# Optimization experiments

Hardware: AMD Instinct MI355X
Metric: run time of the kernel (lower is better)

The kernel has to match this reference:

```python
import jax, jax.numpy as jnp
import numpy as np
import math

DIM = 1024
HEADS = 16
HEAD_DIM = DIM // HEADS
FFN = 4096
B, S = 2, 2048
EPS = 1e-12


def layernorm(x, w, b):
    u = jnp.mean(x, axis=-1, keepdims=True)
    s = jnp.mean((x - u) ** 2, axis=-1, keepdims=True)
    return w * ((x - u) / jnp.sqrt(s + EPS)) + b


def setup_inputs() -> dict:
    key = jax.random.key(0)
    ks = jax.random.split(key, 8)
    scale = 0.02
    return {
        "x": jax.random.normal(ks[0], (B, S, DIM), dtype=jnp.float32),
        "mask": jnp.zeros((1, 1, S, S), dtype=jnp.float32),
        "wq": jax.random.normal(ks[1], (DIM, DIM), dtype=jnp.float32) * scale,
        "wk": jax.random.normal(ks[2], (DIM, DIM), dtype=jnp.float32) * scale,
        "wv": jax.random.normal(ks[3], (DIM, DIM), dtype=jnp.float32) * scale,
        "wo": jax.random.normal(ks[4], (DIM, DIM), dtype=jnp.float32) * scale,
        "w1": jax.random.normal(ks[5], (DIM, FFN), dtype=jnp.float32) * scale,
        "w2": jax.random.normal(ks[6], (FFN, DIM), dtype=jnp.float32) * scale,
        "ln1_w": jnp.ones((DIM,), dtype=jnp.float32),
        "ln1_b": jnp.zeros((DIM,), dtype=jnp.float32),
        "ln2_w": jnp.ones((DIM,), dtype=jnp.float32),
        "ln2_b": jnp.zeros((DIM,), dtype=jnp.float32),
    }


def reference(x, mask, wq, wk, wv, wo, w1, w2, ln1_w, ln1_b, ln2_w, ln2_b):
    # --- attention sub-block (pre-LN) ---
    h = layernorm(x, ln1_w, ln1_b)
    q = (h @ wq).reshape(B, S, HEADS, HEAD_DIM).transpose(0, 2, 1, 3)  # [B,H,S,D]
    k = (h @ wk).reshape(B, S, HEADS, HEAD_DIM).transpose(0, 2, 1, 3)
    v = (h @ wv).reshape(B, S, HEADS, HEAD_DIM).transpose(0, 2, 1, 3)
    scores = jnp.einsum("bhsd,bhtd->bhst", q, k) / math.sqrt(HEAD_DIM)
    scores = scores + mask
    probs = jax.nn.softmax(scores.astype(jnp.float32), axis=-1).astype(q.dtype)
    attn = jnp.einsum("bhst,bhtd->bhsd", probs, v)  # [B,H,S,D]
    attn = attn.transpose(0, 2, 1, 3).reshape(B, S, DIM)
    x = x + attn @ wo
    # --- FFN sub-block (pre-LN) ---
    h = layernorm(x, ln2_w, ln2_b)
    m = jax.nn.gelu(h @ w1, approximate=False) @ w2
    return x + m
```

## Files before the change

kernel.cpp:

```cpp
#include <hip/hip_runtime.h>
#include <math.h>


#define DIMSZ 1024
#define SEQ   2048
#define BATCH 2
#define NHEAD 16
#define HD    64
#define FFNSZ 4096
#define ROWS  (BATCH*SEQ)

typedef __attribute__((ext_vector_type(8))) short bf8_t;
typedef __attribute__((ext_vector_type(4))) float f4_t;

__device__ __forceinline__ unsigned short f2bf(float f) {
  union { float f; unsigned u; } c; c.f = f;
  unsigned u = c.u;
  return (unsigned short)((u + 0x7fffu + ((u >> 16) & 1u)) >> 16);
}

__device__ __forceinline__ float fast_exp2(float x) {
#if __has_builtin(__builtin_amdgcn_exp2f)
  return __builtin_amdgcn_exp2f(x);
#else
  return exp2f(x);
#endif
}

__device__ __forceinline__ unsigned int pk_trunc_bf16(float a, float b) {
#if __has_builtin(__builtin_amdgcn_perm)
  return __builtin_amdgcn_perm(__float_as_uint(b), __float_as_uint(a), 0x07060302u);
#else
  return (__float_as_uint(b) & 0xffff0000u) | (__float_as_uint(a) >> 16);
#endif
}

__device__ __forceinline__ void async16(const void* g, void* l) {
  __builtin_amdgcn_global_load_lds((const __attribute__((address_space(1))) void*)g,
                                   (__attribute__((address_space(3))) void*)l,
                                   16, 0, 0);
}

__device__ __forceinline__ f4_t mfma_bf16(bf8_t a, bf8_t b, f4_t c) {
  return __builtin_amdgcn_mfma_f32_16x16x32_bf16(a, b, c, 0, 0, 0);
}

__global__ __launch_bounds__(256) void ln_kernel(const float* __restrict__ x,
                                                 const float* __restrict__ w,
                                                 const float* __restrict__ b,
                                                 unsigned short* __restrict__ out) {
  int row  = blockIdx.x * 4 + (threadIdx.x >> 6);
  int lane = threadIdx.x & 63;
  const float4* xr = (const float4*)(x + (size_t)row * DIMSZ);
  float4 v[4];
  float s = 0.f, s2 = 0.f;
#pragma unroll
  for (int i = 0; i < 4; ++i) {
    v[i] = xr[lane + 64*i];
    s  += (v[i].x + v[i].y) + (v[i].z + v[i].w);
    s2 += (v[i].x*v[i].x + v[i].y*v[i].y) + (v[i].z*v[i].z + v[i].w*v[i].w);
  }
#pragma unroll
  for (int off = 32; off; off >>= 1) {
    s  += __shfl_xor(s,  off);
    s2 += __shfl_xor(s2, off);
  }
  float mean = s * (1.f/DIMSZ);
  float var  = s2 * (1.f/DIMSZ) - mean*mean;
  float rstd = rsqrtf(var + 1e-12f);
  const float4* wr = (const float4*)w;
  const float4* br = (const float4*)b;
#pragma unroll
  for (int i = 0; i < 4; ++i) {
    float4 wv = wr[lane + 64*i];
    float4 bv = br[lane + 64*i];
    ushort4 o;
    o.x = f2bf((v[i].x - mean) * rstd * wv.x + bv.x);
    o.y = f2bf((v[i].y - mean) * rstd * wv.y + bv.y);
    o.z = f2bf((v[i].z - mean) * rstd * wv.z + bv.z);
    o.w = f2bf((v[i].w - mean) * rstd * wv.w + bv.w);
    *(ushort4*)(out + (size_t)row * DIMSZ + (size_t)(lane + 64*i) * 4) = o;
  }
}

__global__ __launch_bounds__(256) void wtrans4_kernel(const float* __restrict__ w0,
                                                      const float* __restrict__ w1,
                                                      const float* __restrict__ w2,
                                                      const float* __restrict__ w3,
                                                      unsigned short* __restrict__ o0,
                                                      unsigned short* __restrict__ o1,
                                                      unsigned short* __restrict__ o2,
                                                      unsigned short* __restrict__ o3) {
  const int K = 1024, N = 1024;
  const float* w = (blockIdx.z == 0) ? w0 : (blockIdx.z == 1) ? w1 : (blockIdx.z == 2) ? w2 : w3;
  unsigned short* wT = (blockIdx.z == 0) ? o0 : (blockIdx.z == 1) ? o1 : (blockIdx.z == 2) ? o2 : o3;
  __shared__ float t[32][33];
  int tx = threadIdx.x & 31, ty = threadIdx.x >> 5;
  int n0 = blockIdx.x * 32, k0 = blockIdx.y * 32;
#pragma unroll
  for (int i = 0; i < 4; ++i)
    t[ty + 8*i][tx] = w[(size_t)(k0 + ty + 8*i) * N + n0 + tx];
  __syncthreads();
#pragma unroll
  for (int i = 0; i < 4; ++i)
    wT[(size_t)(n0 + ty + 8*i) * K + k0 + tx] = f2bf(t[tx][ty + 8*i]);
}

__global__ __launch_bounds__(256) void wtrans_kernel(const float* __restrict__ w,
                                                     unsigned short* __restrict__ wT,
                                                     int K, int N) {
  __shared__ float t[32][33];
  int tx = threadIdx.x & 31, ty = threadIdx.x >> 5;
  int n0 = blockIdx.x * 32, k0 = blockIdx.y * 32;
#pragma unroll
  for (int i = 0; i < 4; ++i)
    t[ty + 8*i][tx] = w[(size_t)(k0 + ty + 8*i) * N + n0 + tx];
  __syncthreads();
#pragma unroll
  for (int i = 0; i < 4; ++i)
    wT[(size_t)(n0 + ty + 8*i) * K + k0 + tx] = f2bf(t[tx][ty + 8*i]);
}

__global__ __launch_bounds__(256) void vt_kernel(const unsigned short* __restrict__ qkv,
                                                 unsigned short* __restrict__ vt) {
  __shared__ unsigned short tile[64][65];
  int bh = blockIdx.y, b = bh >> 4, h = bh & 15;
  int s0 = blockIdx.x * 64;
  int tx = threadIdx.x & 63, ty = threadIdx.x >> 6;
#pragma unroll
  for (int i = 0; i < 16; ++i) {
    int s = ty + i*4;
    tile[s][tx] = qkv[((size_t)(b*SEQ) + s0 + s) * 3072 + 2048 + h*HD + tx];
  }
  __syncthreads();
#pragma unroll
  for (int i = 0; i < 16; ++i) {
    int d = ty + i*4;
    vt[((size_t)bh * HD + d) * SEQ + s0 + tx] = tile[tx][d];
  }
}

template<int EPI>
__global__ __launch_bounds__(256) void gemm_bt(const unsigned short* __restrict__ A,
                                               const unsigned short* __restrict__ Bt,
                                               void* __restrict__ Cv,
                                               const float* __restrict__ res,
                                               int M, int N, int K) {
  __shared__ unsigned short As[128*32];
  __shared__ unsigned short Bs[128*32];
  int tid  = threadIdx.x;
  int wv   = tid >> 6, lane = tid & 63, quad = lane >> 4, ml = lane & 15;
  int wrow = (wv >> 1) * 64, wcol = (wv & 1) * 64;
  const unsigned short* Ab = A  + (size_t)blockIdx.y * 128 * K;
  const unsigned short* Bb = Bt + (size_t)blockIdx.x * 128 * K;

  f4_t acc[4][4];
#pragma unroll
  for (int i = 0; i < 4; ++i)
#pragma unroll
    for (int j = 0; j < 4; ++j) acc[i][j] = (f4_t){0.f, 0.f, 0.f, 0.f};

  int r0 = tid >> 2, c0 = (tid & 3) * 8;

  for (int k0 = 0; k0 < K; k0 += 32) {
    async16(Ab + (size_t)r0 * K + k0 + c0,        &As[(size_t)tid * 8]);
    async16(Ab + (size_t)(r0+64) * K + k0 + c0,   &As[((size_t)tid + 256) * 8]);
    async16(Bb + (size_t)r0 * K + k0 + c0,        &Bs[(size_t)tid * 8]);
    async16(Bb + (size_t)(r0+64) * K + k0 + c0,   &Bs[((size_t)tid + 256) * 8]);
    __syncthreads();

    bf8_t af[4], bfr[4];
#pragma unroll
    for (int i = 0; i < 4; ++i)
      af[i] = *(const bf8_t*)(&As[(wrow + i*16 + ml) * 32 + quad * 8]);
#pragma unroll
    for (int j = 0; j < 4; ++j)
      bfr[j] = *(const bf8_t*)(&Bs[(wcol + j*16 + ml) * 32 + quad * 8]);
#pragma unroll
    for (int i = 0; i < 4; ++i)
#pragma unroll
      for (int j = 0; j < 4; ++j)
        acc[i][j] = mfma_bf16(af[i], bfr[j], acc[i][j]);
    __syncthreads();
  }

#pragma unroll
  for (int i = 0; i < 4; ++i) {
    int grow = blockIdx.y * 128 + wrow + i*16 + quad*4;
#pragma unroll
    for (int j = 0; j < 4; ++j) {
      int gcol = blockIdx.x * 128 + wcol + j*16 + ml;
#pragma unroll
      for (int r = 0; r < 4; ++r) {
        size_t off = (size_t)(grow + r) * N + gcol;
        float v = acc[i][j][r];
        if constexpr (EPI == 2) {
          ((float*)Cv)[off] = res[off] + v;
        } else {
          if constexpr (EPI == 1)
            v = 0.5f * v * (1.f + erff(v * 0.70710678118654752f));
          ((unsigned short*)Cv)[off] = f2bf(v);
        }
      }
    }
  }
}

__global__ __launch_bounds__(256) void attn_kernel(const unsigned short* __restrict__ qkv,
                                                   const unsigned short* __restrict__ vt,
                                                   const float* __restrict__ mask,
                                                   unsigned short* __restrict__ attnout) {
  __shared__ unsigned short Ks[2][2][64][32];
  __shared__ unsigned short Vs[2][2][64][32];
  __shared__ unsigned short Ps[4][16][72];

  int bh = blockIdx.y, b = bh >> 4, h = bh & 15;
  int tid = threadIdx.x;
  int wv = tid >> 6, lane = tid & 63;
  int quad = lane >> 4, ml = lane & 15;
  int q0 = blockIdx.x * 64;
  int q  = q0 + wv * 16 + ml;

  const unsigned short* qrow = qkv + ((size_t)(b*SEQ) + q) * 3072 + h*HD;
  bf8_t qf0 = *(const bf8_t*)(qrow + quad*8);
  bf8_t qf1 = *(const bf8_t*)(qrow + 32 + quad*8);

  const unsigned short* kbase = qkv + (size_t)(b*SEQ) * 3072 + DIMSZ + h*HD;
  const unsigned short* vbase = vt + (size_t)bh * HD * SEQ;
  const float* mrow = mask + (size_t)q * SEQ;

  int srow = tid >> 2;
  int scol = (tid & 3) * 8;

  f4_t O[4];
#pragma unroll
  for (int dt = 0; dt < 4; ++dt) O[dt] = (f4_t){0.f, 0.f, 0.f, 0.f};
  float lR = 0.f;

  const float C1 = 0.18033688011112042f;
  const float C2 = 1.4426950408889634f;

  auto stage = [&](int t0, int buf) {
#pragma unroll
    for (int dh = 0; dh < 2; ++dh)
      async16(kbase + (size_t)(t0 + srow) * 3072 + dh*32 + scol,
              &Ks[buf][dh][0][0] + (size_t)tid * 8);
#pragma unroll
    for (int kc = 0; kc < 2; ++kc)
      async16(vbase + (size_t)srow * SEQ + t0 + kc*32 + scol,
              &Vs[buf][kc][0][0] + (size_t)tid * 8);
  };
  auto loadmask = [&](int t0, float4* mv) {
#pragma unroll
    for (int mt = 0; mt < 4; ++mt)
      mv[mt] = *(const float4*)(mrow + t0 + mt*16 + quad*4);
  };
  auto compute = [&](int buf, const float4* mv) {
#pragma unroll
    for (int mt = 0; mt < 4; ++mt) {
      bf8_t kf0 = *(const bf8_t*)(&Ks[buf][0][mt*16 + ml][quad*8]);
      bf8_t kf1 = *(const bf8_t*)(&Ks[buf][1][mt*16 + ml][quad*8]);
      f4_t s = (f4_t){0.f, 0.f, 0.f, 0.f};
      s = mfma_bf16(kf0, qf0, s);
      s = mfma_bf16(kf1, qf1, s);
      float p0 = fast_exp2(fmaf(s[0], C1, mv[mt].x * C2));
      float p1 = fast_exp2(fmaf(s[1], C1, mv[mt].y * C2));
      float p2 = fast_exp2(fmaf(s[2], C1, mv[mt].z * C2));
      float p3 = fast_exp2(fmaf(s[3], C1, mv[mt].w * C2));
      lR += (p0 + p1) + (p2 + p3);
      uint2 pk;
      pk.x = pk_trunc_bf16(p0, p1);
      pk.y = pk_trunc_bf16(p2, p3);
      *(uint2*)(&Ps[wv][ml][mt*16 + quad*4]) = pk;
    }
#pragma unroll
    for (int kc = 0; kc < 2; ++kc) {
      bf8_t pf = *(const bf8_t*)(&Ps[wv][ml][kc*32 + quad*8]);
#pragma unroll
      for (int dt = 0; dt < 4; ++dt) {
        bf8_t vf = *(const bf8_t*)(&Vs[buf][kc][dt*16 + ml][quad*8]);
        O[dt] = mfma_bf16(vf, pf, O[dt]);
      }
    }
  };

  float4 mcur[4], mnxt[4];
  stage(0, 0);
  loadmask(0, mcur);

#pragma unroll 1
  for (int c = 0; c < SEQ/64; c += 2) {
    __syncthreads();
    loadmask((c+1)*64, mnxt);
    stage((c+1)*64, 1);
    compute(0, mcur);
    __syncthreads();
    if (c + 2 < SEQ/64) {
      loadmask((c+2)*64, mcur);
      stage((c+2)*64, 0);
    }
    compute(1, mnxt);
  }

  lR += __shfl_xor(lR, 16);
  lR += __shfl_xor(lR, 32);
  float linv = 1.f / lR;
#pragma unroll
  for (int dt = 0; dt < 4; ++dt) {
    ushort4 o;
    o.x = f2bf(O[dt][0] * linv);
    o.y = f2bf(O[dt][1] * linv);
    o.z = f2bf(O[dt][2] * linv);
    o.w = f2bf(O[dt][3] * linv);
    *(ushort4*)(attnout + ((size_t)(b*SEQ) + q) * DIMSZ + h*HD + dt*16 + quad*4) = o;
  }
}

extern "C" void kernel_launch(void* const* d_in, const int* in_sizes, int n_in,
                              void* d_out, int out_size, void* d_ws, size_t ws_size,
                              hipStream_t stream) {
  const float* x    = (const float*)d_in[0];
  const float* mask = (const float*)d_in[1];
  const float* wq   = (const float*)d_in[2];
  const float* wk   = (const float*)d_in[3];
  const float* wvp  = (const float*)d_in[4];
  const float* wo   = (const float*)d_in[5];
  const float* w1   = (const float*)d_in[6];
  const float* w2   = (const float*)d_in[7];
  const float* ln1w = (const float*)d_in[8];
  const float* ln1b = (const float*)d_in[9];
  const float* ln2w = (const float*)d_in[10];
  const float* ln2b = (const float*)d_in[11];
  float* out = (float*)d_out;

  char* ws = (char*)d_ws;
  unsigned short* wqkvT  = (unsigned short*)(ws + 0);
  unsigned short* woT    = (unsigned short*)(ws + 6291456);
  unsigned short* w1T    = (unsigned short*)(ws + 8388608);
  unsigned short* w2T    = (unsigned short*)(ws + 16777216);
  unsigned short* attno  = (unsigned short*)(ws + 25165824);
  float*          x2     = (float*)         (ws + 33554432);
  unsigned short* hbuf   = (unsigned short*)(ws + 50331648);
  unsigned short* qkvb   = (unsigned short*)(ws + 58720256);
  unsigned short* vtb    = (unsigned short*)(ws + 83886080);
  unsigned short* gbuf   = (unsigned short*)(ws + 58720256);

  ln_kernel<<<ROWS/4, 256, 0, stream>>>(x, ln1w, ln1b, hbuf);
  wtrans4_kernel<<<dim3(32, 32, 4), 256, 0, stream>>>(wq, wk, wvp, wo,
      wqkvT, wqkvT + 1024*1024, wqkvT + 2*1024*1024, woT);
  wtrans_kernel<<<dim3(128, 32), 256, 0, stream>>>(w1, w1T, 1024, 4096);
  wtrans_kernel<<<dim3(32, 128), 256, 0, stream>>>(w2, w2T, 4096, 1024);
  gemm_bt<0><<<dim3(3072/128, 4096/128), 256, 0, stream>>>(hbuf, wqkvT, qkvb, nullptr, ROWS, 3072, 1024);
  vt_kernel<<<dim3(SEQ/64, BATCH*NHEAD), 256, 0, stream>>>(qkvb, vtb);
  attn_kernel<<<dim3(SEQ/64, BATCH*NHEAD), 256, 0, stream>>>(qkvb, vtb, mask, attno);
  gemm_bt<2><<<dim3(1024/128, 4096/128), 256, 0, stream>>>(attno, woT, x2, x, ROWS, 1024, 1024);
  ln_kernel<<<ROWS/4, 256, 0, stream>>>(x2, ln2w, ln2b, hbuf);
  gemm_bt<1><<<dim3(4096/128, 4096/128), 256, 0, stream>>>(hbuf, w1T, gbuf, nullptr, ROWS, FFNSZ, 1024);
  gemm_bt<2><<<dim3(1024/128, 4096/128), 256, 0, stream>>>(gbuf, w2T, out, x2, ROWS, 1024, 4096);

  (void)in_sizes; (void)n_in; (void)out_size; (void)ws_size;
}
```

Before: 477.6 us.

## Templatize GEMM N-tile, deepen K step, vectorize epilogue, simplify attention loop

The GEMM gains a template N-tile size, and the two N=1024 projections use 64-wide tiles to launch more blocks. Each iteration now loads a 64-wide K slab, halving the barriers per K, and the MFMA operands are swapped so each lane holds four consecutive columns. That lets the epilogue use float4 and ushort4 stores instead of scalar stores. The attention kernel drops its double-buffered K/V prefetch for a single-buffer loop with two barriers per tile, which removes load/compute overlap there and may slow it.

```diff
diff --git a/kernel.cpp b/kernel.cpp
--- a/kernel.cpp
+++ b/kernel.cpp
@@ -140,67 +140,86 @@
   }
 }
 
-template<int EPI>
+template<int EPI, int NT>
 __global__ __launch_bounds__(256) void gemm_bt(const unsigned short* __restrict__ A,
                                                const unsigned short* __restrict__ Bt,
                                                void* __restrict__ Cv,
                                                const float* __restrict__ res,
                                                int M, int N, int K) {
-  __shared__ unsigned short As[128*32];
-  __shared__ unsigned short Bs[128*32];
+  constexpr int JT = NT / 32;
+  __shared__ unsigned short As[2][128][32];
+  __shared__ unsigned short Bs[2][NT][32];
   int tid  = threadIdx.x;
   int wv   = tid >> 6, lane = tid & 63, quad = lane >> 4, ml = lane & 15;
-  int wrow = (wv >> 1) * 64, wcol = (wv & 1) * 64;
+  int wrow = (wv >> 1) * 64, wcol = (wv & 1) * (NT/2);
   const unsigned short* Ab = A  + (size_t)blockIdx.y * 128 * K;
-  const unsigned short* Bb = Bt + (size_t)blockIdx.x * 128 * K;
-
-  f4_t acc[4][4];
-#pragma unroll
-  for (int i = 0; i < 4; ++i)
-#pragma unroll
-    for (int j = 0; j < 4; ++j) acc[i][j] = (f4_t){0.f, 0.f, 0.f, 0.f};
+  const unsigned short* Bb = Bt + (size_t)blockIdx.x * NT  * K;
+
+  f4_t acc[4][JT];
+#pragma unroll
+  for (int i = 0; i < 4; ++i)
+#pragma unroll
+    for (int j = 0; j < JT; ++j) acc[i][j] = (f4_t){0.f, 0.f, 0.f, 0.f};
 
   int r0 = tid >> 2, c0 = (tid & 3) * 8;
 
-  for (int k0 = 0; k0 < K; k0 += 32) {
-    async16(Ab + (size_t)r0 * K + k0 + c0,        &As[(size_t)tid * 8]);
-    async16(Ab + (size_t)(r0+64) * K + k0 + c0,   &As[((size_t)tid + 256) * 8]);
-    async16(Bb + (size_t)r0 * K + k0 + c0,        &Bs[(size_t)tid * 8]);
-    async16(Bb + (size_t)(r0+64) * K + k0 + c0,   &Bs[((size_t)tid + 256) * 8]);
+  for (int k0 = 0; k0 < K; k0 += 64) {
+#pragma unroll
+    for (int h = 0; h < 2; ++h) {
+      const unsigned short* ap = Ab + (size_t)r0 * K + k0 + h*32 + c0;
+      async16(ap,          &As[h][r0][c0]);
+      async16(ap + 64*K,   &As[h][r0 + 64][c0]);
+      const unsigned short* bp = Bb + (size_t)r0 * K + k0 + h*32 + c0;
+      async16(bp,          &Bs[h][r0][c0]);
+      if constexpr (NT == 128)
+        async16(bp + 64*K, &Bs[h][r0 + 64][c0]);
+    }
     __syncthreads();
 
-    bf8_t af[4], bfr[4];
-#pragma unroll
-    for (int i = 0; i < 4; ++i)
-      af[i] = *(const bf8_t*)(&As[(wrow + i*16 + ml) * 32 + quad * 8]);
-#pragma unroll
-    for (int j = 0; j < 4; ++j)
-      bfr[j] = *(const bf8_t*)(&Bs[(wcol + j*16 + ml) * 32 + quad * 8]);
-#pragma unroll
-    for (int i = 0; i < 4; ++i)
-#pragma unroll
-      for (int j = 0; j < 4; ++j)
-        acc[i][j] = mfma_bf16(af[i], bfr[j], acc[i][j]);
+#pragma unroll
+    for (int h = 0; h < 2; ++h) {
+      bf8_t af[4], bfr[JT];
+#pragma unroll
+      for (int i = 0; i < 4; ++i)
+        af[i] = *(const bf8_t*)(&As[h][wrow + i*16 + ml][quad * 8]);
+#pragma unroll
+      for (int j = 0; j < JT; ++j)
+        bfr[j] = *(const bf8_t*)(&Bs[h][wcol + j*16 + ml][quad * 8]);
+#pragma unroll
+      for (int i = 0; i < 4; ++i)
+#pragma unroll
+        for (int j = 0; j < JT; ++j)
+          acc[i][j] = mfma_bf16(bfr[j], af[i], acc[i][j]);
+    }
     __syncthreads();
   }
 
 #pragma unroll
   for (int i = 0; i < 4; ++i) {
-    int grow = blockIdx.y * 128 + wrow + i*16 + quad*4;
-#pragma unroll
-    for (int j = 0; j < 4; ++j) {
-      int gcol = blockIdx.x * 128 + wcol + j*16 + ml;
-#pragma unroll
-      for (int r = 0; r < 4; ++r) {
-        size_t off = (size_t)(grow + r) * N + gcol;
-        float v = acc[i][j][r];
-        if constexpr (EPI == 2) {
-          ((float*)Cv)[off] = res[off] + v;
-        } else {
-          if constexpr (EPI == 1)
-            v = 0.5f * v * (1.f + erff(v * 0.70710678118654752f));
-          ((unsigned short*)Cv)[off] = f2bf(v);
+    int m = blockIdx.y * 128 + wrow + i*16 + ml;
+#pragma unroll
+    for (int j = 0; j < JT; ++j) {
+      int n = blockIdx.x * NT + wcol + j*16 + quad*4;
+      size_t off = (size_t)m * N + n;
+      if constexpr (EPI == 2) {
+        float4 rv = *(const float4*)(res + off);
+        float4 ov;
+        ov.x = rv.x + acc[i][j][0];
+        ov.y = rv.y + acc[i][j][1];
+        ov.z = rv.z + acc[i][j][2];
+        ov.w = rv.w + acc[i][j][3];
+        *(float4*)((float*)Cv + off) = ov;
+      } else {
+        float v0 = acc[i][j][0], v1 = acc[i][j][1], v2 = acc[i][j][2], v3 = acc[i][j][3];
+        if constexpr (EPI == 1) {
+          v0 = 0.5f * v0 * (1.f + erff(v0 * 0.70710678118654752f));
+          v1 = 0.5f * v1 * (1.f + erff(v1 * 0.70710678118654752f));
+          v2 = 0.5f * v2 * (1.f + erff(v2 * 0.70710678118654752f));
+          v3 = 0.5f * v3 * (1.f + erff(v3 * 0.70710678118654752f));
         }
+        ushort4 o;
+        o.x = f2bf(v0); o.y = f2bf(v1); o.z = f2bf(v2); o.w = f2bf(v3);
+        *(ushort4*)((unsigned short*)Cv + off) = o;
       }
     }
   }
@@ -210,8 +229,8 @@
                                                    const unsigned short* __restrict__ vt,
                                                    const float* __restrict__ mask,
                                                    unsigned short* __restrict__ attnout) {
-  __shared__ unsigned short Ks[2][2][64][32];
-  __shared__ unsigned short Vs[2][2][64][32];
+  __shared__ unsigned short Ks[2][64][32];
+  __shared__ unsigned short Vs[2][64][32];
   __shared__ unsigned short Ps[4][16][72];
 
   int bh = blockIdx.y, b = bh >> 4, h = bh & 15;
@@ -240,26 +259,27 @@
   const float C1 = 0.18033688011112042f;
   const float C2 = 1.4426950408889634f;
 
-  auto stage = [&](int t0, int buf) {
+  for (int t0 = 0; t0 < SEQ; t0 += 64) {
+    float4 mv[4];
+#pragma unroll
+    for (int mt = 0; mt < 4; ++mt)
+      mv[mt] = *(const float4*)(mrow + t0 + mt*16 + quad*4);
+
+    __syncthreads();
 #pragma unroll
     for (int dh = 0; dh < 2; ++dh)
       async16(kbase + (size_t)(t0 + srow) * 3072 + dh*32 + scol,
-              &Ks[buf][dh][0][0] + (size_t)tid * 8);
+              &Ks[dh][0][0] + (size_t)tid * 8);
 #pragma unroll
     for (int kc = 0; kc < 2; ++kc)
       async16(vbase + (size_t)srow * SEQ + t0 + kc*32 + scol,
-              &Vs[buf][kc][0][0] + (size_t)tid * 8);
-  };
-  auto loadmask = [&](int t0, float4* mv) {
-#pragma unroll
-    for (int mt = 0; mt < 4; ++mt)
-      mv[mt] = *(const float4*)(mrow + t0 + mt*16 + quad*4);
-  };
-  auto compute = [&](int buf, const float4* mv) {
+              &Vs[kc][0][0] + (size_t)tid * 8);
+    __syncthreads();
+
 #pragma unroll
     for (int mt = 0; mt < 4; ++mt) {
-      bf8_t kf0 = *(const bf8_t*)(&Ks[buf][0][mt*16 + ml][quad*8]);
-      bf8_t kf1 = *(const bf8_t*)(&Ks[buf][1][mt*16 + ml][quad*8]);
+      bf8_t kf0 = *(const bf8_t*)(&Ks[0][mt*16 + ml][quad*8]);
+      bf8_t kf1 = *(const bf8_t*)(&Ks[1][mt*16 + ml][quad*8]);
       f4_t s = (f4_t){0.f, 0.f, 0.f, 0.f};
       s = mfma_bf16(kf0, qf0, s);
       s = mfma_bf16(kf1, qf1, s);
@@ -273,33 +293,16 @@
       pk.y = pk_trunc_bf16(p2, p3);
       *(uint2*)(&Ps[wv][ml][mt*16 + quad*4]) = pk;
     }
+
 #pragma unroll
     for (int kc = 0; kc < 2; ++kc) {
       bf8_t pf = *(const bf8_t*)(&Ps[wv][ml][kc*32 + quad*8]);
 #pragma unroll
       for (int dt = 0; dt < 4; ++dt) {
-        bf8_t vf = *(const bf8_t*)(&Vs[buf][kc][dt*16 + ml][quad*8]);
+        bf8_t vf = *(const bf8_t*)(&Vs[kc][dt*16 + ml][quad*8]);
         O[dt] = mfma_bf16(vf, pf, O[dt]);
       }
     }
-  };
-
-  float4 mcur[4], mnxt[4];
-  stage(0, 0);
-  loadmask(0, mcur);
-
-#pragma unroll 1
-  for (int c = 0; c < SEQ/64; c += 2) {
-    __syncthreads();
-    loadmask((c+1)*64, mnxt);
-    stage((c+1)*64, 1);
-    compute(0, mcur);
-    __syncthreads();
-    if (c + 2 < SEQ/64) {
-      loadmask((c+2)*64, mcur);
-      stage((c+2)*64, 0);
-    }
-    compute(1, mnxt);
   }
 
   lR += __shfl_xor(lR, 16);
@@ -350,13 +353,13 @@
       wqkvT, wqkvT + 1024*1024, wqkvT + 2*1024*1024, woT);
   wtrans_kernel<<<dim3(128, 32), 256, 0, stream>>>(w1, w1T, 1024, 4096);
   wtrans_kernel<<<dim3(32, 128), 256, 0, stream>>>(w2, w2T, 4096, 1024);
-  gemm_bt<0><<<dim3(3072/128, 4096/128), 256, 0, stream>>>(hbuf, wqkvT, qkvb, nullptr, ROWS, 3072, 1024);
+  gemm_bt<0,128><<<dim3(3072/128, 4096/128), 256, 0, stream>>>(hbuf, wqkvT, qkvb, nullptr, ROWS, 3072, 1024);
   vt_kernel<<<dim3(SEQ/64, BATCH*NHEAD), 256, 0, stream>>>(qkvb, vtb);
   attn_kernel<<<dim3(SEQ/64, BATCH*NHEAD), 256, 0, stream>>>(qkvb, vtb, mask, attno);
-  gemm_bt<2><<<dim3(1024/128, 4096/128), 256, 0, stream>>>(attno, woT, x2, x, ROWS, 1024, 1024);
+  gemm_bt<2,64><<<dim3(1024/64, 4096/128), 256, 0, stream>>>(attno, woT, x2, x, ROWS, 1024, 1024);
   ln_kernel<<<ROWS/4, 256, 0, stream>>>(x2, ln2w, ln2b, hbuf);
-  gemm_bt<1><<<dim3(4096/128, 4096/128), 256, 0, stream>>>(hbuf, w1T, gbuf, nullptr, ROWS, FFNSZ, 1024);
-  gemm_bt<2><<<dim3(1024/128, 4096/128), 256, 0, stream>>>(gbuf, w2T, out, x2, ROWS, 1024, 4096);
+  gemm_bt<1,128><<<dim3(4096/128, 4096/128), 256, 0, stream>>>(hbuf, w1T, gbuf, nullptr, ROWS, FFNSZ, 1024);
+  gemm_bt<2,64><<<dim3(1024/64, 4096/128), 256, 0, stream>>>(gbuf, w2T, out, x2, ROWS, 1024, 4096);
 
   (void)in_sizes; (void)n_in; (void)out_size; (void)ws_size;
 }
```

Measured after the change: 424.1 us. 1.13x faster.
